# Performance work log

Measured on AMD Instinct MI355X. Metric: run time of the kernel, lower is better.

Reference implementation:

```python
import jax, jax.numpy as jnp
import numpy as np

nT, nB, nC = 128, 256, 512      # encoder timesteps, batch, feature channels (= input_size)
H = 512                          # hidden_size
L = 26                           # decode steps per sample (uniform text_length)
NCLS = 6736                      # num_classes


def setup_inputs() -> dict:
    key = jax.random.key(0)
    ks = jax.random.split(key, 12)
    g = lambda k, shp, s: (jax.random.normal(k, shp, jnp.float32) * s)
    return {
        "feats": jax.random.normal(ks[0], (nT, nB, nC), jnp.float32),
        "text_length": jnp.full((nB,), L, dtype=jnp.int32),
        # AttentionCell params (torch Linear weight layout: [out, in])
        "W_i2h": g(ks[1], (H, nC), 0.04),          # i2h, no bias
        "W_h2h": g(ks[2], (H, H), 0.04),
        "b_h2h": g(ks[3], (H,), 0.04),
        "W_score": g(ks[4], (1, H), 0.04),          # score, no bias
        # GRUCell params, gate order r,z,n
        "W_ih": g(ks[5], (3 * H, nC), 0.04),
        "W_hh": g(ks[6], (3 * H, H), 0.04),
        "b_ih": g(ks[7], (3 * H,), 0.04),
        "b_hh": g(ks[8], (3 * H,), 0.04),
        # generator
        "W_gen": g(ks[9], (NCLS, H), 0.04),
        "b_gen": g(ks[10], (NCLS,), 0.04),
    }


def reference(feats, text_length, W_i2h, W_h2h, b_h2h, W_score, W_ih, W_hh,
              b_ih, b_hh, W_gen, b_gen):
    T, B, C = feats.shape
    steps = int(np.asarray(text_length).max())  # uniform lengths -> static loop count

    # i2h(feats) does not depend on the hidden state: precompute once.
    feats_proj = jnp.einsum('tbc,hc->tbh', feats, W_i2h)  # [T,B,H]
    w_score = W_score[0]                                   # [H]

    def step(h, _):
        # Bahdanau attention (original runs per-sample with nB==1; batched here)
        hp = h @ W_h2h.T + b_h2h                           # [B,H]
        e = jnp.einsum('tbh,h->tb', jnp.tanh(feats_proj + hp[None]), w_score)
        alpha = jax.nn.softmax(e, axis=0)                  # softmax over T (nB==1 case)
        context = jnp.einsum('tb,tbc->bc', alpha, feats)   # [B,C]
        # GRUCell(context, h), torch gate order r,z,n
        gi = context @ W_ih.T + b_ih                       # [B,3H]
        gh = h @ W_hh.T + b_hh                             # [B,3H]
        ir, iz, i_n = jnp.split(gi, 3, axis=1)
        hr, hz, h_n = jnp.split(gh, 3, axis=1)
        r = jax.nn.sigmoid(ir + hr)
        z = jax.nn.sigmoid(iz + hz)
        n = jnp.tanh(i_n + r * h_n)
        h_new = (1.0 - z) * n + z * h
        return h_new, h_new

    h0 = jnp.zeros((B, W_h2h.shape[0]), feats.dtype)
    _, hs = jax.lax.scan(step, h0, None, length=steps)     # [steps,B,H]

    # original fills output_hiddens with k = j*L + i ordering (batch outer, step inner)
    out_h = hs.transpose(1, 0, 2).reshape(B * steps, -1)   # [num_labels,H]
    probs = out_h @ W_gen.T + b_gen                        # [num_labels,NCLS]
    return probs
```

## Files before the change

kernel.cpp:

```cpp
#include <hip/hip_runtime.h>

#define T_   128
#define B_   256
#define C_   512
#define H_   512
#define L_   26
#define NCLS 6736
#define NPAD 6784

typedef __attribute__((ext_vector_type(8))) short short8;
typedef __attribute__((ext_vector_type(4))) float f32x4;

__device__ __forceinline__ unsigned short f2b(float f) {
    union { float f; unsigned int u; } v; v.f = f;
    unsigned int r = (v.u + 0x7fffu + ((v.u >> 16) & 1u)) >> 16;
    return (unsigned short)r;
}
__device__ __forceinline__ float b2f(unsigned short u) {
    union { unsigned int u; float f; } v; v.u = ((unsigned int)u) << 16;
    return v.f;
}
__device__ __forceinline__ float tanh_fast(float x) {
    float e = __expf(2.f * x);
    return 1.f - 2.f / (e + 1.f);
}
__device__ __forceinline__ float sigm(float x) {
    return 1.f / (1.f + __expf(-x));
}
__device__ __forceinline__ void llds16(const unsigned short* g, unsigned short* l) {
    __builtin_amdgcn_global_load_lds(
        (const __attribute__((address_space(1))) void*)g,
        (__attribute__((address_space(3))) void*)l, 16, 0, 0);
}

__global__ __launch_bounds__(256) void prep_kernel(
    const float* __restrict__ feats, const float* __restrict__ W_i2h,
    const float* __restrict__ W_gen, const float* __restrict__ W_h2h,
    const float* __restrict__ W_hh, const float* __restrict__ W_ih,
    unsigned short* __restrict__ feats16, unsigned short* __restrict__ wi2h16,
    unsigned short* __restrict__ wgen16, unsigned short* __restrict__ w1_16,
    unsigned short* __restrict__ wih16,
    float* __restrict__ h32, unsigned short* __restrict__ h16)
{
    size_t idx = (size_t)blockIdx.x * 256 + threadIdx.x;
    feats16[idx] = f2b(feats[idx]);
    if (idx < (size_t)H_ * C_) wi2h16[idx] = f2b(W_i2h[idx]);
    if (idx < (size_t)NPAD * H_)
        wgen16[idx] = (idx < (size_t)NCLS * H_) ? f2b(W_gen[idx]) : (unsigned short)0;
    if (idx < (size_t)2048 * 512)
        w1_16[idx] = f2b(idx < 262144 ? W_h2h[idx] : W_hh[idx - 262144]);
    if (idx < (size_t)1536 * 512) wih16[idx] = f2b(W_ih[idx]);
    if (idx < (size_t)B_ * H_) { h32[idx] = 0.f; h16[idx] = 0; }
}

template<int OUTMODE>
__global__ __launch_bounds__(256) void gemm_bt(
    const unsigned short* __restrict__ A, const unsigned short* __restrict__ B,
    void* __restrict__ outp, const float* __restrict__ bias,
    int M, int N, int K, int ncols)
{
    __shared__ unsigned short As[128 * 32];
    __shared__ unsigned short Bs[128 * 32];
    const int tid = threadIdx.x;
    const int lane = tid & 63;

    const int gridN = (int)gridDim.x, gridM = (int)gridDim.y;
    const int bid = (int)blockIdx.y * gridN + (int)blockIdx.x;
    const int GM = 8;
    const int per = GM * gridN;
    const int grp = bid / per;
    const int rem = bid - grp * per;
    const int gsz0 = gridM - grp * GM;
    const int gsz = gsz0 < GM ? gsz0 : GM;
    const int m0 = (grp * GM + rem % gsz) * 128;
    const int n0 = (rem / gsz) * 128;

    const int wv = tid >> 6;
    const int wm = (wv >> 1) * 64;
    const int wn = (wv & 1) * 64;

    f32x4 acc[4][4];
#pragma unroll
    for (int i = 0; i < 4; i++)
#pragma unroll
        for (int j = 0; j < 4; j++) acc[i][j] = (f32x4)0.f;

    for (int k0 = 0; k0 < K; k0 += 32) {
        __syncthreads();
#pragma unroll
        for (int is = 0; is < 2; ++is) {
            int c = is * 256 + tid;
            int row = c >> 2, col = (c & 3) * 8;
            llds16(A + (size_t)(m0 + row) * K + k0 + col, &As[c * 8]);
            llds16(B + (size_t)(n0 + row) * K + k0 + col, &Bs[c * 8]);
        }
        __syncthreads();
        short8 af[4], bf[4];
#pragma unroll
        for (int t = 0; t < 4; t++) {
            af[t] = *(const short8*)&As[(wm + t * 16 + (lane & 15)) * 32 + (lane >> 4) * 8];
            bf[t] = *(const short8*)&Bs[(wn + t * 16 + (lane & 15)) * 32 + (lane >> 4) * 8];
        }
#pragma unroll
        for (int i = 0; i < 4; i++)
#pragma unroll
            for (int j = 0; j < 4; j++)
                acc[i][j] = __builtin_amdgcn_mfma_f32_16x16x32_bf16(af[i], bf[j], acc[i][j], 0, 0, 0);
    }

    const int cr = (lane >> 4) * 4;
    const int cc = lane & 15;
    if constexpr (OUTMODE == 0) {
        unsigned short* o = (unsigned short*)outp;
#pragma unroll
        for (int i = 0; i < 4; i++)
#pragma unroll
            for (int j = 0; j < 4; j++) {
                int col = n0 + wn + j * 16 + cc;
#pragma unroll
                for (int r = 0; r < 4; r++) {
                    int row = m0 + wm + i * 16 + cr + r;
                    o[(size_t)row * N + col] = f2b(acc[i][j][r]);
                }
            }
    } else {
        float* o = (float*)outp;
#pragma unroll
        for (int j = 0; j < 4; j++) {
            int col = n0 + wn + j * 16 + cc;
            if (col < ncols) {
                float bv = bias[col];
#pragma unroll
                for (int i = 0; i < 4; i++)
#pragma unroll
                    for (int r = 0; r < 4; r++) {
                        int row = m0 + wm + i * 16 + cr + r;
                        o[(size_t)row * ncols + col] = acc[i][j][r] + bv;
                    }
            }
        }
    }
}

__global__ __launch_bounds__(256) void gemm_hg(
    const unsigned short* __restrict__ h16, const unsigned short* __restrict__ w1,
    const float* __restrict__ b_h2h, const float* __restrict__ b_hh,
    float* __restrict__ hp, float* __restrict__ gh)
{
    const int tid = threadIdx.x, lane = tid & 63, wv = tid >> 6;
    const int m0 = blockIdx.y * 16;
    const int n0 = blockIdx.x * 128 + wv * 32;
    const unsigned short* ap = h16 + (size_t)(m0 + (lane & 15)) * H_ + (lane >> 4) * 8;
    const unsigned short* bp = w1 + (size_t)(n0 + (lane & 15)) * H_ + (lane >> 4) * 8;
    f32x4 acc0 = (f32x4)0.f, acc1 = (f32x4)0.f;
#pragma unroll
    for (int k0 = 0; k0 < H_; k0 += 32) {
        short8 a  = *(const short8*)(ap + k0);
        short8 b0 = *(const short8*)(bp + k0);
        short8 b1 = *(const short8*)(bp + (size_t)16 * H_ + k0);
        acc0 = __builtin_amdgcn_mfma_f32_16x16x32_bf16(a, b0, acc0, 0, 0, 0);
        acc1 = __builtin_amdgcn_mfma_f32_16x16x32_bf16(a, b1, acc1, 0, 0, 0);
    }
    const int cc = lane & 15, cr = (lane >> 4) * 4;
#pragma unroll
    for (int j = 0; j < 2; j++) {
        int col = n0 + j * 16 + cc;
        f32x4 av = j ? acc1 : acc0;
        float bv = (col < H_) ? b_h2h[col] : b_hh[col - H_];
#pragma unroll
        for (int r = 0; r < 4; r++) {
            int row = m0 + cr + r;
            float v = av[r] + bv;
            if (col < H_) hp[(size_t)row * H_ + col] = v;
            else          gh[(size_t)row * 1536 + (col - H_)] = v;
        }
    }
}

__global__ __launch_bounds__(1024) void attn_fused(
    const unsigned short* __restrict__ fp, const unsigned short* __restrict__ feats16,
    const float* __restrict__ hp, const float* __restrict__ wscore,
    unsigned short* __restrict__ ctx16)
{
    const int b = blockIdx.x;
    const int tid = threadIdx.x, lane = tid & 63, wv = tid >> 6;
    __shared__ float se[T_];
    __shared__ float ctx4[4][C_];

    float hpr[8], wsr[8];
    {
        const float* hb = hp + b * H_ + lane * 8;
        const float* wb = wscore + lane * 8;
#pragma unroll
        for (int i = 0; i < 8; i++) { hpr[i] = hb[i]; wsr[i] = wb[i]; }
    }
#pragma unroll
    for (int i = 0; i < 8; i++) {
        int t = wv * 8 + i;
        short8 v = *(const short8*)(fp + ((size_t)t * B_ + b) * H_ + lane * 8);
        float p = 0.f;
#pragma unroll
        for (int j = 0; j < 8; j++)
            p += wsr[j] * tanh_fast(b2f((unsigned short)v[j]) + hpr[j]);
#pragma unroll
        for (int off = 32; off > 0; off >>= 1) p += __shfl_xor(p, off, 64);
        if (lane == 0) se[t] = p;
    }
    __syncthreads();
    if (wv == 0) {
        float v0 = se[lane], v1 = se[lane + 64];
        float mx = fmaxf(v0, v1);
#pragma unroll
        for (int off = 32; off > 0; off >>= 1) mx = fmaxf(mx, __shfl_xor(mx, off, 64));
        float e0 = __expf(v0 - mx), e1 = __expf(v1 - mx);
        float s = e0 + e1;
#pragma unroll
        for (int off = 32; off > 0; off >>= 1) s += __shfl_xor(s, off, 64);
        float inv = 1.f / s;
        se[lane] = e0 * inv; se[lane + 64] = e1 * inv;
    }
    __syncthreads();
    const int c = (tid & 255) * 2;
    const int q = tid >> 8;
    float a0 = 0.f, a1 = 0.f;
    const unsigned short* fb = feats16 + (size_t)b * C_ + c;
    for (int i = 0; i < 32; i++) {
        int t = q * 32 + i;
        float al = se[t];
        unsigned int u = *(const unsigned int*)(fb + (size_t)t * B_ * C_);
        a0 += al * b2f((unsigned short)(u & 0xffffu));
        a1 += al * b2f((unsigned short)(u >> 16));
    }
    ctx4[q][c] = a0; ctx4[q][c + 1] = a1;
    __syncthreads();
    if (tid < C_) {
        float s = ctx4[0][tid] + ctx4[1][tid] + ctx4[2][tid] + ctx4[3][tid];
        ctx16[(size_t)b * C_ + tid] = f2b(s);
    }
}

__global__ __launch_bounds__(256) void gemm_gates(
    const unsigned short* __restrict__ ctx, const unsigned short* __restrict__ wih,
    const float* __restrict__ gh, const float* __restrict__ b_ih,
    const float* __restrict__ hin32, float* __restrict__ hout32,
    unsigned short* __restrict__ hout16, unsigned short* __restrict__ outH, int step)
{
    const int tid = threadIdx.x, lane = tid & 63, wv = tid >> 6;
    const int m0 = blockIdx.y * 16;
    const int n0 = blockIdx.x * 64 + wv * 16;
    const unsigned short* ap = ctx + (size_t)(m0 + (lane & 15)) * C_ + (lane >> 4) * 8;
    const unsigned short* bp = wih + (size_t)(n0 + (lane & 15)) * H_ + (lane >> 4) * 8;
    f32x4 ar = (f32x4)0.f, az = (f32x4)0.f, an = (f32x4)0.f;
#pragma unroll
    for (int k0 = 0; k0 < H_; k0 += 32) {
        short8 a  = *(const short8*)(ap + k0);
        short8 br = *(const short8*)(bp + k0);
        short8 bz = *(const short8*)(bp + (size_t)512 * H_ + k0);
        short8 bn = *(const short8*)(bp + (size_t)1024 * H_ + k0);
        ar = __builtin_amdgcn_mfma_f32_16x16x32_bf16(a, br, ar, 0, 0, 0);
        az = __builtin_amdgcn_mfma_f32_16x16x32_bf16(a, bz, az, 0, 0, 0);
        an = __builtin_amdgcn_mfma_f32_16x16x32_bf16(a, bn, an, 0, 0, 0);
    }
    const int cc = lane & 15, cr = (lane >> 4) * 4;
    const int col = n0 + cc;
    const float br_ = b_ih[col], bz_ = b_ih[512 + col], bn_ = b_ih[1024 + col];
#pragma unroll
    for (int r = 0; r < 4; r++) {
        int row = m0 + cr + r;
        float ghr = gh[(size_t)row * 1536 + col];
        float ghz = gh[(size_t)row * 1536 + 512 + col];
        float ghn = gh[(size_t)row * 1536 + 1024 + col];
        float hv  = hin32[(size_t)row * H_ + col];
        float rg = sigm(ar[r] + br_ + ghr);
        float zg = sigm(az[r] + bz_ + ghz);
        float ng = tanh_fast(an[r] + bn_ + rg * ghn);
        float hn = (1.f - zg) * ng + zg * hv;
        hout32[(size_t)row * H_ + col] = hn;
        unsigned short hb = f2b(hn);
        hout16[(size_t)row * H_ + col] = hb;
        outH[((size_t)row * L_ + step) * H_ + col] = hb;
    }
}

extern "C" void kernel_launch(void* const* d_in, const int* in_sizes, int n_in,
                              void* d_out, int out_size, void* d_ws, size_t ws_size,
                              hipStream_t stream)
{
    const float* feats   = (const float*)d_in[0];
    const float* W_i2h   = (const float*)d_in[2];
    const float* W_h2h   = (const float*)d_in[3];
    const float* b_h2h   = (const float*)d_in[4];
    const float* W_score = (const float*)d_in[5];
    const float* W_ih    = (const float*)d_in[6];
    const float* W_hh    = (const float*)d_in[7];
    const float* b_ih    = (const float*)d_in[8];
    const float* b_hh    = (const float*)d_in[9];
    const float* W_gen   = (const float*)d_in[10];
    const float* b_gen   = (const float*)d_in[11];

    char* ws = (char*)d_ws;
    size_t off = 0;
    auto alloc = [&](size_t bytes) {
        void* p = ws + off; off += (bytes + 255) & ~(size_t)255; return p;
    };
    unsigned short* feats16 = (unsigned short*)alloc((size_t)T_ * B_ * C_ * 2);
    unsigned short* fp16    = (unsigned short*)alloc((size_t)T_ * B_ * H_ * 2);
    unsigned short* wgen16  = (unsigned short*)alloc((size_t)NPAD * H_ * 2);
    unsigned short* wi2h16  = (unsigned short*)alloc((size_t)H_ * C_ * 2);
    unsigned short* w1_16   = (unsigned short*)alloc((size_t)2048 * 512 * 2);
    unsigned short* wih16   = (unsigned short*)alloc((size_t)1536 * 512 * 2);
    unsigned short* outH16  = (unsigned short*)alloc((size_t)B_ * L_ * H_ * 2);
    float* h32a = (float*)alloc((size_t)B_ * H_ * 4);
    float* h32b = (float*)alloc((size_t)B_ * H_ * 4);
    unsigned short* h16a = (unsigned short*)alloc((size_t)B_ * H_ * 2);
    unsigned short* h16b = (unsigned short*)alloc((size_t)B_ * H_ * 2);
    float* hp  = (float*)alloc((size_t)B_ * H_ * 4);
    float* gh  = (float*)alloc((size_t)B_ * 1536 * 4);
    unsigned short* ctx16 = (unsigned short*)alloc((size_t)B_ * C_ * 2);

    prep_kernel<<<dim3((T_ * B_ * C_) / 256), 256, 0, stream>>>(
        feats, W_i2h, W_gen, W_h2h, W_hh, W_ih,
        feats16, wi2h16, wgen16, w1_16, wih16, h32a, h16a);

    gemm_bt<0><<<dim3(H_ / 128, (T_ * B_) / 128), 256, 0, stream>>>(
        feats16, wi2h16, fp16, nullptr, T_ * B_, H_, C_, 0);

    for (int s = 0; s < L_; s++) {
        const float* hin32          = (s & 1) ? h32b : h32a;
        float* hout32               = (s & 1) ? h32a : h32b;
        const unsigned short* hin16 = (s & 1) ? h16b : h16a;
        unsigned short* hout16      = (s & 1) ? h16a : h16b;
        gemm_hg<<<dim3(16, 16), 256, 0, stream>>>(hin16, w1_16, b_h2h, b_hh, hp, gh);
        attn_fused<<<dim3(B_), 1024, 0, stream>>>(fp16, feats16, hp, W_score, ctx16);
        gemm_gates<<<dim3(8, 16), 256, 0, stream>>>(
            ctx16, wih16, gh, b_ih, hin32, hout32, hout16, outH16, s);
    }

    gemm_bt<1><<<dim3(NPAD / 128, (B_ * L_) / 128), 256, 0, stream>>>(
        outH16, wgen16, d_out, b_gen, B_ * L_, NPAD, H_, NCLS);
}
```

Before: 1.338 ms.

## Fuse hidden projections into attention and gate kernels, dropping separate h-GEMM

Removes the per-step gemm_hg launch. Each attention block now computes its own h@W_h2h^T row with scalar FMAs over a transposed bf16 W_h2h, and the gate kernel computes h@W_hh^T with extra MFMAs next to the context GEMM. This cuts one launch per decode step and the round trip of hp and gh through global memory. In exchange each of the 256 attention blocks re-reads the full 512x512 W_h2h, with scalar math instead of MFMA, and the gate kernel's per-block work doubles.

```diff
diff --git a/kernel.cpp b/kernel.cpp
--- a/kernel.cpp
+++ b/kernel.cpp
@@ -38,8 +38,8 @@
     const float* __restrict__ W_gen, const float* __restrict__ W_h2h,
     const float* __restrict__ W_hh, const float* __restrict__ W_ih,
     unsigned short* __restrict__ feats16, unsigned short* __restrict__ wi2h16,
-    unsigned short* __restrict__ wgen16, unsigned short* __restrict__ w1_16,
-    unsigned short* __restrict__ wih16,
+    unsigned short* __restrict__ wgen16, unsigned short* __restrict__ w2hT16,
+    unsigned short* __restrict__ whh16, unsigned short* __restrict__ wih16,
     float* __restrict__ h32, unsigned short* __restrict__ h16)
 {
     size_t idx = (size_t)blockIdx.x * 256 + threadIdx.x;
@@ -47,9 +47,12 @@
     if (idx < (size_t)H_ * C_) wi2h16[idx] = f2b(W_i2h[idx]);
     if (idx < (size_t)NPAD * H_)
         wgen16[idx] = (idx < (size_t)NCLS * H_) ? f2b(W_gen[idx]) : (unsigned short)0;
-    if (idx < (size_t)2048 * 512)
-        w1_16[idx] = f2b(idx < 262144 ? W_h2h[idx] : W_hh[idx - 262144]);
-    if (idx < (size_t)1536 * 512) wih16[idx] = f2b(W_ih[idx]);
+    if (idx < (size_t)H_ * H_)
+        w2hT16[idx] = f2b(W_h2h[(idx & 511) * 512 + (idx >> 9)]);
+    if (idx < (size_t)1536 * 512) {
+        whh16[idx] = f2b(W_hh[idx]);
+        wih16[idx] = f2b(W_ih[idx]);
+    }
     if (idx < (size_t)B_ * H_) { h32[idx] = 0.f; h16[idx] = 0; }
 }
 
@@ -142,55 +145,43 @@
     }
 }
 
-__global__ __launch_bounds__(256) void gemm_hg(
-    const unsigned short* __restrict__ h16, const unsigned short* __restrict__ w1,
-    const float* __restrict__ b_h2h, const float* __restrict__ b_hh,
-    float* __restrict__ hp, float* __restrict__ gh)
-{
-    const int tid = threadIdx.x, lane = tid & 63, wv = tid >> 6;
-    const int m0 = blockIdx.y * 16;
-    const int n0 = blockIdx.x * 128 + wv * 32;
-    const unsigned short* ap = h16 + (size_t)(m0 + (lane & 15)) * H_ + (lane >> 4) * 8;
-    const unsigned short* bp = w1 + (size_t)(n0 + (lane & 15)) * H_ + (lane >> 4) * 8;
-    f32x4 acc0 = (f32x4)0.f, acc1 = (f32x4)0.f;
-#pragma unroll
-    for (int k0 = 0; k0 < H_; k0 += 32) {
-        short8 a  = *(const short8*)(ap + k0);
-        short8 b0 = *(const short8*)(bp + k0);
-        short8 b1 = *(const short8*)(bp + (size_t)16 * H_ + k0);
-        acc0 = __builtin_amdgcn_mfma_f32_16x16x32_bf16(a, b0, acc0, 0, 0, 0);
-        acc1 = __builtin_amdgcn_mfma_f32_16x16x32_bf16(a, b1, acc1, 0, 0, 0);
-    }
-    const int cc = lane & 15, cr = (lane >> 4) * 4;
-#pragma unroll
-    for (int j = 0; j < 2; j++) {
-        int col = n0 + j * 16 + cc;
-        f32x4 av = j ? acc1 : acc0;
-        float bv = (col < H_) ? b_h2h[col] : b_hh[col - H_];
-#pragma unroll
-        for (int r = 0; r < 4; r++) {
-            int row = m0 + cr + r;
-            float v = av[r] + bv;
-            if (col < H_) hp[(size_t)row * H_ + col] = v;
-            else          gh[(size_t)row * 1536 + (col - H_)] = v;
-        }
-    }
-}
-
-__global__ __launch_bounds__(1024) void attn_fused(
+__global__ __launch_bounds__(1024) void attn_mega(
     const unsigned short* __restrict__ fp, const unsigned short* __restrict__ feats16,
-    const float* __restrict__ hp, const float* __restrict__ wscore,
+    const unsigned short* __restrict__ h16, const unsigned short* __restrict__ w2hT,
+    const float* __restrict__ b_h2h, const float* __restrict__ wscore,
     unsigned short* __restrict__ ctx16)
 {
     const int b = blockIdx.x;
     const int tid = threadIdx.x, lane = tid & 63, wv = tid >> 6;
     __shared__ float se[T_];
     __shared__ float ctx4[4][C_];
+    __shared__ float shp[H_];
+    __shared__ float shh[H_];
+
+    if (tid < H_) shh[tid] = b2f(h16[(size_t)b * H_ + tid]);
+    __syncthreads();
+
+    {
+        const int col = tid & (H_ - 1);
+        const int kh = tid >> 9;
+        const unsigned short* wp = w2hT + (size_t)(kh << 8) * H_ + col;
+        const float* hh = &shh[kh << 8];
+        float a0 = 0.f, a1 = 0.f;
+#pragma unroll 8
+        for (int k = 0; k < 256; k += 2) {
+            a0 += hh[k]     * b2f(wp[(size_t)k * H_]);
+            a1 += hh[k + 1] * b2f(wp[(size_t)(k + 1) * H_]);
+        }
+        ctx4[kh][col] = a0 + a1;
+    }
+    __syncthreads();
+    if (tid < H_) shp[tid] = ctx4[0][tid] + ctx4[1][tid] + b_h2h[tid];
+    __syncthreads();
 
     float hpr[8], wsr[8];
     {
-        const float* hb = hp + b * H_ + lane * 8;
         const float* wb = wscore + lane * 8;
+        const float* hb = &shp[lane * 8];
 #pragma unroll
         for (int i = 0; i < 8; i++) { hpr[i] = hb[i]; wsr[i] = wb[i]; }
     }
@@ -239,41 +230,50 @@
     }
 }
 
-__global__ __launch_bounds__(256) void gemm_gates(
+__global__ __launch_bounds__(256) void gates_mega(
     const unsigned short* __restrict__ ctx, const unsigned short* __restrict__ wih,
-    const float* __restrict__ gh, const float* __restrict__ b_ih,
+    const unsigned short* __restrict__ hin16, const unsigned short* __restrict__ whh,
+    const float* __restrict__ b_ih, const float* __restrict__ b_hh,
     const float* __restrict__ hin32, float* __restrict__ hout32,
     unsigned short* __restrict__ hout16, unsigned short* __restrict__ outH, int step)
 {
     const int tid = threadIdx.x, lane = tid & 63, wv = tid >> 6;
     const int m0 = blockIdx.y * 16;
     const int n0 = blockIdx.x * 64 + wv * 16;
-    const unsigned short* ap = ctx + (size_t)(m0 + (lane & 15)) * C_ + (lane >> 4) * 8;
+    const unsigned short* ap = ctx   + (size_t)(m0 + (lane & 15)) * C_ + (lane >> 4) * 8;
+    const unsigned short* ah = hin16 + (size_t)(m0 + (lane & 15)) * H_ + (lane >> 4) * 8;
     const unsigned short* bp = wih + (size_t)(n0 + (lane & 15)) * H_ + (lane >> 4) * 8;
+    const unsigned short* bh = whh + (size_t)(n0 + (lane & 15)) * H_ + (lane >> 4) * 8;
     f32x4 ar = (f32x4)0.f, az = (f32x4)0.f, an = (f32x4)0.f;
+    f32x4 gr = (f32x4)0.f, gz = (f32x4)0.f, gn = (f32x4)0.f;
 #pragma unroll
     for (int k0 = 0; k0 < H_; k0 += 32) {
         short8 a  = *(const short8*)(ap + k0);
+        short8 a2 = *(const short8*)(ah + k0);
         short8 br = *(const short8*)(bp + k0);
         short8 bz = *(const short8*)(bp + (size_t)512 * H_ + k0);
         short8 bn = *(const short8*)(bp + (size_t)1024 * H_ + k0);
-        ar = __builtin_amdgcn_mfma_f32_16x16x32_bf16(a, br, ar, 0, 0, 0);
-        az = __builtin_amdgcn_mfma_f32_16x16x32_bf16(a, bz, az, 0, 0, 0);
-        an = __builtin_amdgcn_mfma_f32_16x16x32_bf16(a, bn, an, 0, 0, 0);
+        short8 cr_ = *(const short8*)(bh + k0);
+        short8 cz_ = *(const short8*)(bh + (size_t)512 * H_ + k0);
+        short8 cn_ = *(const short8*)(bh + (size_t)1024 * H_ + k0);
+        ar = __builtin_amdgcn_mfma_f32_16x16x32_bf16(a,  br,  ar, 0, 0, 0);
+        az = __builtin_amdgcn_mfma_f32_16x16x32_bf16(a,  bz,  az, 0, 0, 0);
+        an = __builtin_amdgcn_mfma_f32_16x16x32_bf16(a,  bn,  an, 0, 0, 0);
+        gr = __builtin_amdgcn_mfma_f32_16x16x32_bf16(a2, cr_, gr, 0, 0, 0);
+        gz = __builtin_amdgcn_mfma_f32_16x16x32_bf16(a2, cz_, gz, 0, 0, 0);
+        gn = __builtin_amdgcn_mfma_f32_16x16x32_bf16(a2, cn_, gn, 0, 0, 0);
     }
     const int cc = lane & 15, cr = (lane >> 4) * 4;
     const int col = n0 + cc;
-    const float br_ = b_ih[col], bz_ = b_ih[512 + col], bn_ = b_ih[1024 + col];
+    const float bir = b_ih[col], biz = b_ih[512 + col], bin = b_ih[1024 + col];
+    const float bhr = b_hh[col], bhz = b_hh[512 + col], bhn = b_hh[1024 + col];
 #pragma unroll
     for (int r = 0; r < 4; r++) {
         int row = m0 + cr + r;
-        float ghr = gh[(size_t)row * 1536 + col];
-        float ghz = gh[(size_t)row * 1536 + 512 + col];
-        float ghn = gh[(size_t)row * 1536 + 1024 + col];
-        float hv  = hin32[(size_t)row * H_ + col];
-        float rg = sigm(ar[r] + br_ + ghr);
-        float zg = sigm(az[r] + bz_ + ghz);
-        float ng = tanh_fast(an[r] + bn_ + rg * ghn);
+        float hv = hin32[(size_t)row * H_ + col];
+        float rg = sigm(ar[r] + bir + gr[r] + bhr);
+        float zg = sigm(az[r] + biz + gz[r] + bhz);
+        float ng = tanh_fast(an[r] + bin + rg * (gn[r] + bhn));
         float hn = (1.f - zg) * ng + zg * hv;
         hout32[(size_t)row * H_ + col] = hn;
         unsigned short hb = f2b(hn);
@@ -307,20 +307,19 @@
     unsigned short* fp16    = (unsigned short*)alloc((size_t)T_ * B_ * H_ * 2);
     unsigned short* wgen16  = (unsigned short*)alloc((size_t)NPAD * H_ * 2);
     unsigned short* wi2h16  = (unsigned short*)alloc((size_t)H_ * C_ * 2);
-    unsigned short* w1_16   = (unsigned short*)alloc((size_t)2048 * 512 * 2);
+    unsigned short* w2hT16  = (unsigned short*)alloc((size_t)H_ * H_ * 2);
+    unsigned short* whh16   = (unsigned short*)alloc((size_t)1536 * 512 * 2);
     unsigned short* wih16   = (unsigned short*)alloc((size_t)1536 * 512 * 2);
     unsigned short* outH16  = (unsigned short*)alloc((size_t)B_ * L_ * H_ * 2);
     float* h32a = (float*)alloc((size_t)B_ * H_ * 4);
     float* h32b = (float*)alloc((size_t)B_ * H_ * 4);
     unsigned short* h16a = (unsigned short*)alloc((size_t)B_ * H_ * 2);
     unsigned short* h16b = (unsigned short*)alloc((size_t)B_ * H_ * 2);
-    float* hp  = (float*)alloc((size_t)B_ * H_ * 4);
-    float* gh  = (float*)alloc((size_t)B_ * 1536 * 4);
     unsigned short* ctx16 = (unsigned short*)alloc((size_t)B_ * C_ * 2);
 
     prep_kernel<<<dim3((T_ * B_ * C_) / 256), 256, 0, stream>>>(
         feats, W_i2h, W_gen, W_h2h, W_hh, W_ih,
-        feats16, wi2h16, wgen16, w1_16, wih16, h32a, h16a);
+        feats16, wi2h16, wgen16, w2hT16, whh16, wih16, h32a, h16a);
 
     gemm_bt<0><<<dim3(H_ / 128, (T_ * B_) / 128), 256, 0, stream>>>(
         feats16, wi2h16, fp16, nullptr, T_ * B_, H_, C_, 0);
@@ -330,10 +329,10 @@
         float* hout32               = (s & 1) ? h32a : h32b;
         const unsigned short* hin16 = (s & 1) ? h16b : h16a;
         unsigned short* hout16      = (s & 1) ? h16a : h16b;
-        gemm_hg<<<dim3(16, 16), 256, 0, stream>>>(hin16, w1_16, b_h2h, b_hh, hp, gh);
-        attn_fused<<<dim3(B_), 1024, 0, stream>>>(fp16, feats16, hp, W_score, ctx16);
-        gemm_gates<<<dim3(8, 16), 256, 0, stream>>>(
-            ctx16, wih16, gh, b_ih, hin32, hout32, hout16, outH16, s);
+        attn_mega<<<dim3(B_), 1024, 0, stream>>>(
+            fp16, feats16, hin16, w2hT16, b_h2h, W_score, ctx16);
+        gates_mega<<<dim3(8, 16), 256, 0, stream>>>(
+            ctx16, wih16, hin16, whh16, b_ih, b_hh, hin32, hout32, hout16, outH16, s);
     }
 
     gemm_bt<1><<<dim3(NPAD / 128, (B_ * L_) / 128), 256, 0, stream>>>(
```

New measurement: 1.516 ms. +13.3%, slower.

## Move h@W_hh GEMM into attention kernel as extra blocks, shrink h2h GEMM

Applied to the files above, without the earlier changes.

Splits the combined h2h/hh GEMM so the first per-step kernel computes only the attention projection hp, which is on the critical path. The gh = h@W_hh^T GEMM is computed by 32 extra 1024-thread blocks appended to the attention kernel, so it runs alongside the attention work. The goal is to shorten the serial launch chain per decode step. In exchange, the attention kernel's block count grows and its resources are shared with the GEMM blocks.

```diff
diff --git a/kernel.cpp b/kernel.cpp
--- a/kernel.cpp
+++ b/kernel.cpp
@@ -142,48 +142,70 @@
     }
 }
 
-__global__ __launch_bounds__(256) void gemm_hg(
+__global__ __launch_bounds__(256) void gemm_hp(
     const unsigned short* __restrict__ h16, const unsigned short* __restrict__ w1,
-    const float* __restrict__ b_h2h, const float* __restrict__ b_hh,
-    float* __restrict__ hp, float* __restrict__ gh)
+    const float* __restrict__ b_h2h, float* __restrict__ hp)
 {
     const int tid = threadIdx.x, lane = tid & 63, wv = tid >> 6;
     const int m0 = blockIdx.y * 16;
-    const int n0 = blockIdx.x * 128 + wv * 32;
+    const int n0 = blockIdx.x * 64 + wv * 16;
     const unsigned short* ap = h16 + (size_t)(m0 + (lane & 15)) * H_ + (lane >> 4) * 8;
     const unsigned short* bp = w1 + (size_t)(n0 + (lane & 15)) * H_ + (lane >> 4) * 8;
-    f32x4 acc0 = (f32x4)0.f, acc1 = (f32x4)0.f;
+    f32x4 acc = (f32x4)0.f;
 #pragma unroll
     for (int k0 = 0; k0 < H_; k0 += 32) {
         short8 a  = *(const short8*)(ap + k0);
         short8 b0 = *(const short8*)(bp + k0);
-        short8 b1 = *(const short8*)(bp + (size_t)16 * H_ + k0);
-        acc0 = __builtin_amdgcn_mfma_f32_16x16x32_bf16(a, b0, acc0, 0, 0, 0);
-        acc1 = __builtin_amdgcn_mfma_f32_16x16x32_bf16(a, b1, acc1, 0, 0, 0);
+        acc = __builtin_amdgcn_mfma_f32_16x16x32_bf16(a, b0, acc, 0, 0, 0);
     }
     const int cc = lane & 15, cr = (lane >> 4) * 4;
-#pragma unroll
-    for (int j = 0; j < 2; j++) {
-        int col = n0 + j * 16 + cc;
-        f32x4 av = j ? acc1 : acc0;
-        float bv = (col < H_) ? b_h2h[col] : b_hh[col - H_];
+    const int col = n0 + cc;
+    const float bv = b_h2h[col];
+#pragma unroll
+    for (int r = 0; r < 4; r++)
+        hp[(size_t)(m0 + cr + r) * H_ + col] = acc[r] + bv;
+}
+
+__global__ __launch_bounds__(1024) void attn_gh(
+    const unsigned short* __restrict__ fp, const unsigned short* __restrict__ feats16,
+    const float* __restrict__ hp, const float* __restrict__ wscore,
+    unsigned short* __restrict__ ctx16,
+    const unsigned short* __restrict__ h16, const unsigned short* __restrict__ whh,
+    const float* __restrict__ b_hh, float* __restrict__ gh)
+{
+    const int tid = threadIdx.x, lane = tid & 63, wv = tid >> 6;
+
+    if (blockIdx.x >= B_) {
+        const int u = ((int)blockIdx.x - B_) * 16 + wv;
+        const int m0 = (u >> 5) * 16;
+        const int n0 = (u & 31) * 16;
+        const unsigned short* ah = h16 + (size_t)(m0 + (lane & 15)) * H_ + (lane >> 4) * 8;
+        const unsigned short* bh = whh + (size_t)(n0 + (lane & 15)) * H_ + (lane >> 4) * 8;
+        f32x4 gr = (f32x4)0.f, gz = (f32x4)0.f, gn = (f32x4)0.f;
+#pragma unroll
+        for (int k0 = 0; k0 < H_; k0 += 32) {
+            short8 a   = *(const short8*)(ah + k0);
+            short8 cr_ = *(const short8*)(bh + k0);
+            short8 cz_ = *(const short8*)(bh + (size_t)512 * H_ + k0);
+            short8 cn_ = *(const short8*)(bh + (size_t)1024 * H_ + k0);
+            gr = __builtin_amdgcn_mfma_f32_16x16x32_bf16(a, cr_, gr, 0, 0, 0);
+            gz = __builtin_amdgcn_mfma_f32_16x16x32_bf16(a, cz_, gz, 0, 0, 0);
+            gn = __builtin_amdgcn_mfma_f32_16x16x32_bf16(a, cn_, gn, 0, 0, 0);
+        }
+        const int cc = lane & 15, cr = (lane >> 4) * 4;
+        const int col = n0 + cc;
+        const float bhr = b_hh[col], bhz = b_hh[512 + col], bhn = b_hh[1024 + col];
 #pragma unroll
         for (int r = 0; r < 4; r++) {
             int row = m0 + cr + r;
-            float v = av[r] + bv;
-            if (col < H_) hp[(size_t)row * H_ + col] = v;
-            else          gh[(size_t)row * 1536 + (col - H_)] = v;
-        }
-    }
-}
-
-__global__ __launch_bounds__(1024) void attn_fused(
-    const unsigned short* __restrict__ fp, const unsigned short* __restrict__ feats16,
-    const float* __restrict__ hp, const float* __restrict__ wscore,
-    unsigned short* __restrict__ ctx16)
-{
+            gh[(size_t)row * 1536 + col]        = gr[r] + bhr;
+            gh[(size_t)row * 1536 + 512 + col]  = gz[r] + bhz;
+            gh[(size_t)row * 1536 + 1024 + col] = gn[r] + bhn;
+        }
+        return;
+    }
+
     const int b = blockIdx.x;
-    const int tid = threadIdx.x, lane = tid & 63, wv = tid >> 6;
     __shared__ float se[T_];
     __shared__ float ctx4[4][C_];
 
@@ -330,8 +352,10 @@
         float* hout32               = (s & 1) ? h32a : h32b;
         const unsigned short* hin16 = (s & 1) ? h16b : h16a;
         unsigned short* hout16      = (s & 1) ? h16a : h16b;
-        gemm_hg<<<dim3(16, 16), 256, 0, stream>>>(hin16, w1_16, b_h2h, b_hh, hp, gh);
-        attn_fused<<<dim3(B_), 1024, 0, stream>>>(fp16, feats16, hp, W_score, ctx16);
+        gemm_hp<<<dim3(8, 16), 256, 0, stream>>>(hin16, w1_16, b_h2h, hp);
+        attn_gh<<<dim3(B_ + 32), 1024, 0, stream>>>(
+            fp16, feats16, hp, W_score, ctx16,
+            hin16, w1_16 + 262144, b_hh, gh);
         gemm_gates<<<dim3(8, 16), 256, 0, stream>>>(
             ctx16, wih16, gh, b_ih, hin32, hout32, hout16, outH16, s);
     }
```

Measured after the change: 1.999 ms. +49.4%, slower.
